# Performance work log

Measured on AMD Instinct MI355X. Metric: run time of the kernel, lower is better.

Reference implementation:

```python
import jax, jax.numpy as jnp
import numpy as np

B, S, D = 16, 1024, 1024

def _xavier_uniform(key, shape, fan_in, fan_out):
    a = float(np.sqrt(6.0 / (fan_in + fan_out)))
    return jax.random.uniform(key, shape, jnp.float32, -a, a)

def setup_inputs() -> dict:
    key = jax.random.key(0)
    ks = jax.random.split(key, 8)
    query = jax.random.normal(ks[0], (B, S, D), jnp.float32)
    key_t = jax.random.normal(ks[1], (B, S, D), jnp.float32)
    value = jax.random.normal(ks[2], (B, S, D), jnp.float32)
    # learned additive attention bias [1, S, S], xavier_uniform init
    attn_bias = _xavier_uniform(ks[3], (1, S, S), S, S)
    # Linear weights (torch nn.Linear default: kaiming-uniform-ish; any init ok for baseline)
    Wq = _xavier_uniform(ks[4], (D, D), D, D)
    bq = jnp.zeros((D,), jnp.float32)
    Wk = _xavier_uniform(ks[5], (D, D), D, D)
    bk = jnp.zeros((D,), jnp.float32)
    return {"query": query, "key": key_t, "value": value,
            "attn_bias": attn_bias, "Wq": Wq, "bq": bq, "Wk": Wk, "bk": bk}

def reference(query, key, value, attn_bias, Wq, bq, Wk, bk):
    # q = query @ Wq^T + bq  (torch Linear convention)
    q = jnp.einsum('bsd,ed->bse', query, Wq) + bq            # [B,S,D]
    k = jnp.einsum('bsd,ed->bse', key, Wk) + bk              # [B,S,D]
    energy = jnp.einsum('bsd,btd->bst', q, k) + attn_bias    # [B,S,S] (bias broadcasts over B)
    attention = jax.nn.softmax(energy, axis=-1)
    out = jnp.einsum('bst,btd->bsd', attention, value)       # value is NOT projected (matches source)
    return (out, attention)
```

## Files before the change

### kernel.cpp

```cpp
#include <hip/hip_runtime.h>


#define AS1 __attribute__((address_space(1)))
#define AS3 __attribute__((address_space(3)))
#define VMCNT(n) asm volatile("s_waitcnt vmcnt(" #n ")" ::: "memory")
#define SBARRIER asm volatile("s_barrier" ::: "memory")

typedef __bf16 bf16;
typedef __bf16 bf16x4 __attribute__((ext_vector_type(4)));
typedef __bf16 bf16x8 __attribute__((ext_vector_type(8)));
typedef float  f32x4  __attribute__((ext_vector_type(4)));

constexpr int BATCH = 16;
constexpr int S = 1024;
constexpr int D = 1024;
constexpr long NBSD = (long)BATCH * S * D;

constexpr int GBM = 256, GBN = 256, GBK = 32;
constexpr int NTK = 1024 / GBK;
constexpr int ARR = GBM * GBK;

__device__ __forceinline__ void stage16(const bf16* src, const bf16* dst) {
  __builtin_amdgcn_global_load_lds((const AS1 void*)src, (AS3 void*)dst, 16, 0, 0);
}

__global__ __launch_bounds__(256) void split_convert(
    const float* __restrict__ in, bf16* __restrict__ hi, bf16* __restrict__ lo, int n4) {
  int i = blockIdx.x * blockDim.x + threadIdx.x;
  int stride = gridDim.x * blockDim.x;
  for (; i < n4; i += stride) {
    f32x4 x = ((const f32x4*)in)[i];
    bf16x4 h, l;
#pragma unroll
    for (int j = 0; j < 4; ++j) {
      float v = x[j];
      bf16 hh = (bf16)v;
      h[j] = hh;
      l[j] = (bf16)(v - (float)hh);
    }
    ((bf16x4*)hi)[i] = h;
    ((bf16x4*)lo)[i] = l;
  }
}

__global__ __launch_bounds__(256) void transpose_convert(
    const float* __restrict__ v, bf16* __restrict__ vT) {
  __shared__ float tile[32][33];
  const int b = blockIdx.z;
  const int t0 = blockIdx.y * 32, d0 = blockIdx.x * 32;
  const int tx = threadIdx.x & 31, ty = threadIdx.x >> 5;
  const float* src = v + (long)b * S * D;
#pragma unroll
  for (int i = 0; i < 4; ++i)
    tile[ty + i * 8][tx] = src[(long)(t0 + ty + i * 8) * D + d0 + tx];
  __syncthreads();
  bf16* dst = vT + (long)b * D * S;
#pragma unroll
  for (int i = 0; i < 4; ++i)
    dst[(long)(d0 + ty + i * 8) * S + t0 + tx] = (bf16)tile[tx][ty + i * 8];
}

template <int EPI>
__global__ __launch_bounds__(512, 2) void gemm8_split(
    const bf16* __restrict__ Ah_g, const bf16* __restrict__ Al_g, long a_bs,
    const bf16* __restrict__ Bh_g, const bf16* __restrict__ Bl_g, long b_bs,
    const float* __restrict__ bias,
    bf16* __restrict__ Ch, bf16* __restrict__ Cl,
    float* __restrict__ Cf, long c_bs) {
  __shared__ bf16 lds[2 * 4 * ARR];

  const int tid = threadIdx.x;
  const int lane = tid & 63, wid = tid >> 6;
  const int wr = wid >> 2, wc = wid & 3;
  const int fr = lane & 15, fq = lane >> 4;
  const int fsw = (fr >> 1) & 3;

  const int w = blockIdx.x;
  const int swz = (w & 7) * 32 + (w >> 3);
  int z, by, bx;
  if constexpr (EPI == 0) { z = 0; by = swz >> 2; bx = swz & 3; }
  else { z = swz >> 4; by = (swz >> 2) & 3; bx = swz & 3; }
  const long brow = (long)by * GBM, bcol = (long)bx * GBN;

  const bf16* A_h = Ah_g + (long)z * a_bs;
  const bf16* A_l = Al_g + (long)z * a_bs;
  const bf16* B_h = Bh_g + (long)z * b_bs;
  const bf16* B_l = Bl_g + (long)z * b_bs;

  const int srow = tid >> 2;
  const int csw = ((tid & 3) ^ ((srow >> 1) & 3)) * 8;
  const long asrc = (brow + srow) * 1024 + csw;
  const long bsrc = (bcol + srow) * 1024 + csw;
  const int dstoff = wid * 512;

  const int aoffb = (wr * 128 + fr) * 32 + (fq ^ fsw) * 8;
  const int boffb = (wc * 64 + fr) * 32 + (fq ^ fsw) * 8;

  f32x4 acc[8][4] = {};

#define STG(slot, arr, base, koff, rr) \
  stage16((base) + (koff) + (long)(rr) * 131072, \
          lds + ((slot) * 4 + (arr)) * ARR + (rr) * 4096 + dstoff)

  STG(0, 0, A_h + asrc, 0, 0); STG(0, 0, A_h + asrc, 0, 1);
  STG(0, 2, B_h + bsrc, 0, 0); STG(0, 2, B_h + bsrc, 0, 1);
  STG(0, 3, B_l + bsrc, 0, 0); STG(0, 3, B_l + bsrc, 0, 1);
  STG(0, 1, A_l + asrc, 0, 0); STG(0, 1, A_l + asrc, 0, 1);

  for (int t = 0; t < NTK; ++t) {
    const int cur = t & 1, nxt = cur ^ 1;
    const bf16* lA_h = lds + (cur * 4 + 0) * ARR;
    const bf16* lA_l = lds + (cur * 4 + 1) * ARR;
    const bf16* lB_h = lds + (cur * 4 + 2) * ARR;
    const bf16* lB_l = lds + (cur * 4 + 3) * ARR;

    if (t + 1 < NTK) {
      const long kn = (long)(t + 1) * GBK;
      STG(nxt, 0, A_h + asrc, kn, 0); STG(nxt, 0, A_h + asrc, kn, 1);
      STG(nxt, 2, B_h + bsrc, kn, 0); STG(nxt, 2, B_h + bsrc, kn, 1);
      STG(nxt, 3, B_l + bsrc, kn, 0); STG(nxt, 3, B_l + bsrc, kn, 1);
      STG(nxt, 1, A_l + asrc, kn, 0); STG(nxt, 1, A_l + asrc, kn, 1);
      VMCNT(8);
    } else {
      VMCNT(0);
    }
    __builtin_amdgcn_sched_barrier(0);
    SBARRIER;

    bf16x8 ah[8], bh[4];
#pragma unroll
    for (int m = 0; m < 8; ++m) ah[m] = *(const bf16x8*)&lA_h[aoffb + m * 512];
#pragma unroll
    for (int n = 0; n < 4; ++n) bh[n] = *(const bf16x8*)&lB_h[boffb + n * 512];
#pragma unroll
    for (int n = 0; n < 4; ++n)
#pragma unroll
      for (int m = 0; m < 8; ++m)
        acc[m][n] = __builtin_amdgcn_mfma_f32_16x16x32_bf16(ah[m], bh[n], acc[m][n], 0, 0, 0);

    bf16x8 bl[4];
#pragma unroll
    for (int n = 0; n < 4; ++n) bl[n] = *(const bf16x8*)&lB_l[boffb + n * 512];
#pragma unroll
    for (int n = 0; n < 4; ++n)
#pragma unroll
      for (int m = 0; m < 8; ++m)
        acc[m][n] = __builtin_amdgcn_mfma_f32_16x16x32_bf16(ah[m], bl[n], acc[m][n], 0, 0, 0);

    bf16x8 al[8];
#pragma unroll
    for (int m = 0; m < 8; ++m) al[m] = *(const bf16x8*)&lA_l[aoffb + m * 512];
#pragma unroll
    for (int n = 0; n < 4; ++n)
#pragma unroll
      for (int m = 0; m < 8; ++m)
        acc[m][n] = __builtin_amdgcn_mfma_f32_16x16x32_bf16(al[m], bh[n], acc[m][n], 0, 0, 0);

    SBARRIER;
  }
#undef STG

  if constexpr (EPI == 0) {
#pragma unroll
    for (int n = 0; n < 4; ++n) {
      const long col = bcol + wc * 64 + n * 16 + fr;
      const float bv = bias[col];
#pragma unroll
      for (int m = 0; m < 8; ++m) {
        const long row0 = brow + wr * 128 + m * 16 + fq * 4;
#pragma unroll
        for (int j = 0; j < 4; ++j) {
          const float c = acc[m][n][j] + bv;
          const bf16 h = (bf16)c;
          const bf16 l = (bf16)(c - (float)h);
          const long idx = (row0 + j) * 1024 + col;
          Ch[idx] = h;
          Cl[idx] = l;
        }
      }
    }
  } else {
    float* Cz = Cf + (long)z * c_bs;
#pragma unroll
    for (int n = 0; n < 4; ++n) {
      const long col = bcol + wc * 64 + n * 16 + fr;
#pragma unroll
      for (int m = 0; m < 8; ++m) {
        const long row0 = brow + wr * 128 + m * 16 + fq * 4;
#pragma unroll
        for (int j = 0; j < 4; ++j) {
          const long row = row0 + j;
          Cz[row * 1024 + col] = acc[m][n][j] + bias[row * 1024 + col];
        }
      }
    }
  }
}

__global__ __launch_bounds__(512, 2) void gemm8_plain(
    const bf16* __restrict__ A_g, long a_bs,
    const bf16* __restrict__ B_g, long b_bs,
    float* __restrict__ C, long c_bs) {
  __shared__ bf16 lds[2 * 2 * ARR];

  const int tid = threadIdx.x;
  const int lane = tid & 63, wid = tid >> 6;
  const int wr = wid >> 2, wc = wid & 3;
  const int fr = lane & 15, fq = lane >> 4;
  const int fsw = (fr >> 1) & 3;

  const int w = blockIdx.x;
  const int swz = (w & 7) * 32 + (w >> 3);
  const int z = swz >> 4, by = (swz >> 2) & 3, bx = swz & 3;
  const long brow = (long)by * GBM, bcol = (long)bx * GBN;

  const bf16* A = A_g + (long)z * a_bs;
  const bf16* B = B_g + (long)z * b_bs;

  const int srow = tid >> 2;
  const int csw = ((tid & 3) ^ ((srow >> 1) & 3)) * 8;
  const long asrc = (brow + srow) * 1024 + csw;
  const long bsrc = (bcol + srow) * 1024 + csw;
  const int dstoff = wid * 512;

  const int aoffb = (wr * 128 + fr) * 32 + (fq ^ fsw) * 8;
  const int boffb = (wc * 64 + fr) * 32 + (fq ^ fsw) * 8;

  f32x4 acc[8][4] = {};

#define STG2(slot, arr, base, koff, rr) \
  stage16((base) + (koff) + (long)(rr) * 131072, \
          lds + ((slot) * 2 + (arr)) * ARR + (rr) * 4096 + dstoff)

  STG2(0, 0, A + asrc, 0, 0); STG2(0, 0, A + asrc, 0, 1);
  STG2(0, 1, B + bsrc, 0, 0); STG2(0, 1, B + bsrc, 0, 1);

  for (int t = 0; t < NTK; ++t) {
    const int cur = t & 1, nxt = cur ^ 1;
    const bf16* lA = lds + (cur * 2 + 0) * ARR;
    const bf16* lB = lds + (cur * 2 + 1) * ARR;

    if (t + 1 < NTK) {
      const long kn = (long)(t + 1) * GBK;
      STG2(nxt, 0, A + asrc, kn, 0); STG2(nxt, 0, A + asrc, kn, 1);
      STG2(nxt, 1, B + bsrc, kn, 0); STG2(nxt, 1, B + bsrc, kn, 1);
      VMCNT(4);
    } else {
      VMCNT(0);
    }
    __builtin_amdgcn_sched_barrier(0);
    SBARRIER;

    bf16x8 ah[8], bh[4];
#pragma unroll
    for (int m = 0; m < 8; ++m) ah[m] = *(const bf16x8*)&lA[aoffb + m * 512];
#pragma unroll
    for (int n = 0; n < 4; ++n) bh[n] = *(const bf16x8*)&lB[boffb + n * 512];
#pragma unroll
    for (int n = 0; n < 4; ++n)
#pragma unroll
      for (int m = 0; m < 8; ++m)
        acc[m][n] = __builtin_amdgcn_mfma_f32_16x16x32_bf16(ah[m], bh[n], acc[m][n], 0, 0, 0);

    SBARRIER;
  }
#undef STG2

  float* Cz = C + (long)z * c_bs;
#pragma unroll
  for (int n = 0; n < 4; ++n) {
    const long col = bcol + wc * 64 + n * 16 + fr;
#pragma unroll
    for (int m = 0; m < 8; ++m) {
      const long row0 = brow + wr * 128 + m * 16 + fq * 4;
#pragma unroll
      for (int j = 0; j < 4; ++j)
        Cz[(row0 + j) * 1024 + col] = acc[m][n][j];
    }
  }
}

__global__ __launch_bounds__(256) void softmax_rows(
    float* __restrict__ attn, bf16* __restrict__ attn_bf) {
  const long row = blockIdx.x;
  float* p = attn + row * 1024;
  const int tid = threadIdx.x, lane = tid & 63, wid = tid >> 6;

  f32x4 x = ((const f32x4*)p)[tid];
  float m = fmaxf(fmaxf(x[0], x[1]), fmaxf(x[2], x[3]));
#pragma unroll
  for (int off = 32; off; off >>= 1) m = fmaxf(m, __shfl_xor(m, off));
  __shared__ float redm[4];
  if (lane == 0) redm[wid] = m;
  __syncthreads();
  m = fmaxf(fmaxf(redm[0], redm[1]), fmaxf(redm[2], redm[3]));

  f32x4 e;
#pragma unroll
  for (int j = 0; j < 4; ++j) e[j] = __expf(x[j] - m);
  float s = e[0] + e[1] + e[2] + e[3];
#pragma unroll
  for (int off = 32; off; off >>= 1) s += __shfl_xor(s, off);
  __shared__ float reds[4];
  if (lane == 0) reds[wid] = s;
  __syncthreads();
  s = reds[0] + reds[1] + reds[2] + reds[3];

  const float inv = 1.0f / s;
  f32x4 r;
  bf16x4 rb;
#pragma unroll
  for (int j = 0; j < 4; ++j) {
    r[j] = e[j] * inv;
    rb[j] = (bf16)r[j];
  }
  ((f32x4*)p)[tid] = r;
  ((bf16x4*)(attn_bf + row * 1024))[tid] = rb;
}

extern "C" void kernel_launch(void* const* d_in, const int* in_sizes, int n_in,
                              void* d_out, int out_size, void* d_ws, size_t ws_size,
                              hipStream_t stream) {
  const float* query     = (const float*)d_in[0];
  const float* key       = (const float*)d_in[1];
  const float* value     = (const float*)d_in[2];
  const float* attn_bias = (const float*)d_in[3];
  const float* Wq        = (const float*)d_in[4];
  const float* bq        = (const float*)d_in[5];
  const float* Wk        = (const float*)d_in[6];
  const float* bk        = (const float*)d_in[7];

  float* out  = (float*)d_out;
  float* attn = out + NBSD;

  bf16* ws    = (bf16*)d_ws;
  bf16* q_hi  = ws;
  bf16* q_lo  = ws + NBSD;
  bf16* k_hi  = ws + 2 * NBSD;
  bf16* k_lo  = ws + 3 * NBSD;
  bf16* Wq_hi = ws + 4 * NBSD;
  bf16* Wq_lo = Wq_hi + (long)D * D;
  bf16* Wk_hi = Wq_lo + (long)D * D;
  bf16* Wk_lo = Wk_hi + (long)D * D;
  bf16* scr   = Wk_lo + (long)D * D;
  bf16* key_hi = scr;
  bf16* key_lo = scr + NBSD;
  bf16* valueT  = scr;
  bf16* attn_bf = scr + NBSD;
  bf16* query_hi = (bf16*)d_out;
  bf16* query_lo = query_hi + NBSD;

  split_convert<<<2048, 256, 0, stream>>>(query, query_hi, query_lo, (int)(NBSD / 4));
  split_convert<<<2048, 256, 0, stream>>>(key, key_hi, key_lo, (int)(NBSD / 4));
  split_convert<<<512, 256, 0, stream>>>(Wq, Wq_hi, Wq_lo, D * D / 4);
  split_convert<<<512, 256, 0, stream>>>(Wk, Wk_hi, Wk_lo, D * D / 4);

  gemm8_split<0><<<256, 512, 0, stream>>>(query_hi, query_lo, 0, Wq_hi, Wq_lo, 0,
                                          bq, q_hi, q_lo, nullptr, 0);
  gemm8_split<0><<<256, 512, 0, stream>>>(key_hi, key_lo, 0, Wk_hi, Wk_lo, 0,
                                          bk, k_hi, k_lo, nullptr, 0);

  transpose_convert<<<dim3(32, 32, 16), 256, 0, stream>>>(value, valueT);

  gemm8_split<1><<<256, 512, 0, stream>>>(q_hi, q_lo, (long)S * D, k_hi, k_lo, (long)S * D,
                                          attn_bias, nullptr, nullptr, attn, (long)S * S);

  softmax_rows<<<BATCH * S, 256, 0, stream>>>(attn, attn_bf);

  gemm8_plain<<<256, 512, 0, stream>>>(attn_bf, (long)S * S, valueT, (long)D * S,
                                       out, (long)S * D);
}
```

Measured before the change: 480.8 us.

## Interleave LDS reads, global prefetch and MFMA clusters in split-bf16 projection GEMM

The projection GEMM's K loop used to stage all next-tile data at the top, then read LDS and issue three blocks of MFMAs. It is now broken into six MFMA clusters, with per-cluster s_setprio and fine-grained lgkmcnt/vmcnt waits. Each cluster overlaps partial LDS fragment loads and a slice of the next tile's global-to-LDS copies, and the next tile's A_h/B_h fragments are preloaded across the loop boundary. The aim is to hide LDS and global latency behind matrix-core work, at the cost of more barriers per iteration and a more fragile wait-count schedule.

```diff
diff --git a/kernel.cpp b/kernel.cpp
--- a/kernel.cpp
+++ b/kernel.cpp
@@ -4,7 +4,9 @@
 #define AS1 __attribute__((address_space(1)))
 #define AS3 __attribute__((address_space(3)))
 #define VMCNT(n) asm volatile("s_waitcnt vmcnt(" #n ")" ::: "memory")
+#define LGKM(n)  asm volatile("s_waitcnt lgkmcnt(" #n ")" ::: "memory")
 #define SBARRIER asm volatile("s_barrier" ::: "memory")
+#define SB0 __builtin_amdgcn_sched_barrier(0)
 
 typedef __bf16 bf16;
 typedef __bf16 bf16x4 __attribute__((ext_vector_type(4)));
@@ -97,68 +99,91 @@
   const int boffb = (wc * 64 + fr) * 32 + (fq ^ fsw) * 8;
 
   f32x4 acc[8][4] = {};
+  bf16x8 ah[8], al[8], bh[4], bl[4];
 
 #define STG(slot, arr, base, koff, rr) \
   stage16((base) + (koff) + (long)(rr) * 131072, \
           lds + ((slot) * 4 + (arr)) * ARR + (rr) * 4096 + dstoff)
+
+#define CLUSTER(AF, BF, N0) \
+  __builtin_amdgcn_s_setprio(1); \
+  _Pragma("unroll") \
+  for (int m = 0; m < 8; ++m) \
+    acc[m][N0] = __builtin_amdgcn_mfma_f32_16x16x32_bf16(AF[m], BF[N0], acc[m][N0], 0, 0, 0); \
+  _Pragma("unroll") \
+  for (int m = 0; m < 8; ++m) \
+    acc[m][N0+1] = __builtin_amdgcn_mfma_f32_16x16x32_bf16(AF[m], BF[N0+1], acc[m][N0+1], 0, 0, 0); \
+  __builtin_amdgcn_s_setprio(0)
 
   STG(0, 0, A_h + asrc, 0, 0); STG(0, 0, A_h + asrc, 0, 1);
   STG(0, 2, B_h + bsrc, 0, 0); STG(0, 2, B_h + bsrc, 0, 1);
   STG(0, 3, B_l + bsrc, 0, 0); STG(0, 3, B_l + bsrc, 0, 1);
   STG(0, 1, A_l + asrc, 0, 0); STG(0, 1, A_l + asrc, 0, 1);
+  VMCNT(4);
+  SBARRIER;
+  {
+    const bf16* lA_h0 = lds;
+    const bf16* lB_h0 = lds + 2 * ARR;
+#pragma unroll
+    for (int m = 0; m < 8; ++m) ah[m] = *(const bf16x8*)&lA_h0[aoffb + m * 512];
+    bh[0] = *(const bf16x8*)&lB_h0[boffb];
+    bh[1] = *(const bf16x8*)&lB_h0[boffb + 512];
+  }
 
   for (int t = 0; t < NTK; ++t) {
     const int cur = t & 1, nxt = cur ^ 1;
-    const bf16* lA_h = lds + (cur * 4 + 0) * ARR;
+    const long kn = (long)(t + 1) * GBK;
+    const bool pf = (t + 1 < NTK);
     const bf16* lA_l = lds + (cur * 4 + 1) * ARR;
     const bf16* lB_h = lds + (cur * 4 + 2) * ARR;
     const bf16* lB_l = lds + (cur * 4 + 3) * ARR;
-
-    if (t + 1 < NTK) {
-      const long kn = (long)(t + 1) * GBK;
+    const bf16* nA_h = lds + (nxt * 4 + 0) * ARR;
+    const bf16* nB_h = lds + (nxt * 4 + 2) * ARR;
+
+    bh[2] = *(const bf16x8*)&lB_h[boffb + 2 * 512];
+    bh[3] = *(const bf16x8*)&lB_h[boffb + 3 * 512];
+    if (pf) {
       STG(nxt, 0, A_h + asrc, kn, 0); STG(nxt, 0, A_h + asrc, kn, 1);
-      STG(nxt, 2, B_h + bsrc, kn, 0); STG(nxt, 2, B_h + bsrc, kn, 1);
-      STG(nxt, 3, B_l + bsrc, kn, 0); STG(nxt, 3, B_l + bsrc, kn, 1);
-      STG(nxt, 1, A_l + asrc, kn, 0); STG(nxt, 1, A_l + asrc, kn, 1);
-      VMCNT(8);
+      VMCNT(2);
     } else {
       VMCNT(0);
     }
-    __builtin_amdgcn_sched_barrier(0);
-    SBARRIER;
-
-    bf16x8 ah[8], bh[4];
-#pragma unroll
-    for (int m = 0; m < 8; ++m) ah[m] = *(const bf16x8*)&lA_h[aoffb + m * 512];
-#pragma unroll
-    for (int n = 0; n < 4; ++n) bh[n] = *(const bf16x8*)&lB_h[boffb + n * 512];
-#pragma unroll
-    for (int n = 0; n < 4; ++n)
-#pragma unroll
-      for (int m = 0; m < 8; ++m)
-        acc[m][n] = __builtin_amdgcn_mfma_f32_16x16x32_bf16(ah[m], bh[n], acc[m][n], 0, 0, 0);
-
-    bf16x8 bl[4];
-#pragma unroll
-    for (int n = 0; n < 4; ++n) bl[n] = *(const bf16x8*)&lB_l[boffb + n * 512];
-#pragma unroll
-    for (int n = 0; n < 4; ++n)
-#pragma unroll
-      for (int m = 0; m < 8; ++m)
-        acc[m][n] = __builtin_amdgcn_mfma_f32_16x16x32_bf16(ah[m], bl[n], acc[m][n], 0, 0, 0);
-
-    bf16x8 al[8];
+    SBARRIER; LGKM(2); SB0;
+    CLUSTER(ah, bh, 0);
+
+    bl[0] = *(const bf16x8*)&lB_l[boffb];
+    bl[1] = *(const bf16x8*)&lB_l[boffb + 512];
+    if (pf) { STG(nxt, 2, B_h + bsrc, kn, 0); STG(nxt, 2, B_h + bsrc, kn, 1); }
+    SBARRIER; LGKM(2); SB0;
+    CLUSTER(ah, bh, 2);
+
+    bl[2] = *(const bf16x8*)&lB_l[boffb + 2 * 512];
+    bl[3] = *(const bf16x8*)&lB_l[boffb + 3 * 512];
+    if (pf) { STG(nxt, 3, B_l + bsrc, kn, 0); STG(nxt, 3, B_l + bsrc, kn, 1); }
+    SBARRIER; LGKM(2); SB0;
+    CLUSTER(ah, bl, 0);
+
 #pragma unroll
     for (int m = 0; m < 8; ++m) al[m] = *(const bf16x8*)&lA_l[aoffb + m * 512];
-#pragma unroll
-    for (int n = 0; n < 4; ++n)
-#pragma unroll
-      for (int m = 0; m < 8; ++m)
-        acc[m][n] = __builtin_amdgcn_mfma_f32_16x16x32_bf16(al[m], bh[n], acc[m][n], 0, 0, 0);
-
-    SBARRIER;
+    if (pf) { STG(nxt, 1, A_l + asrc, kn, 0); STG(nxt, 1, A_l + asrc, kn, 1); }
+    SBARRIER; LGKM(8); SB0;
+    CLUSTER(ah, bl, 2);
+
+    if (pf) { VMCNT(4); } else { VMCNT(0); }
+    SBARRIER; LGKM(0); SB0;
+    CLUSTER(al, bh, 0);
+
+    if (pf) {
+#pragma unroll
+      for (int m = 0; m < 8; ++m) ah[m] = *(const bf16x8*)&nA_h[aoffb + m * 512];
+      bh[0] = *(const bf16x8*)&nB_h[boffb];
+      bh[1] = *(const bf16x8*)&nB_h[boffb + 512];
+    }
+    SBARRIER; SB0;
+    CLUSTER(al, bh, 2);
   }
 #undef STG
+#undef CLUSTER
 
   if constexpr (EPI == 0) {
 #pragma unroll
@@ -248,7 +273,7 @@
     } else {
       VMCNT(0);
     }
-    __builtin_amdgcn_sched_barrier(0);
+    SB0;
     SBARRIER;
 
     bf16x8 ah[8], bh[4];
```

Result: faster. 460.6 us (-4.2%).

## Switch split-bf16 GEMM to 32x32x16 MFMA with per-phase staged prefetch

Applied to the files above, without the earlier changes.

Rewrites the three-pass split-bf16 GEMM to use 32x32x16 MFMA tiles instead of 16x16x32, which cuts LDS fragment reads per MFMA. It also staggers the next tile's global-to-LDS prefetch across the three hi/lo MFMA phases, with finer vmcnt/lgkmcnt waits and barriers, and raises wave priority around the MFMA clusters. The aim is better MFMA throughput and overlap of loads with compute. It adds more barriers per k-step and changes the register footprint.

```diff
diff --git a/kernel.cpp b/kernel.cpp
--- a/kernel.cpp
+++ b/kernel.cpp
@@ -4,12 +4,15 @@
 #define AS1 __attribute__((address_space(1)))
 #define AS3 __attribute__((address_space(3)))
 #define VMCNT(n) asm volatile("s_waitcnt vmcnt(" #n ")" ::: "memory")
+#define LGKM(n)  asm volatile("s_waitcnt lgkmcnt(" #n ")" ::: "memory")
 #define SBARRIER asm volatile("s_barrier" ::: "memory")
+#define SB0 __builtin_amdgcn_sched_barrier(0)
 
 typedef __bf16 bf16;
 typedef __bf16 bf16x4 __attribute__((ext_vector_type(4)));
 typedef __bf16 bf16x8 __attribute__((ext_vector_type(8)));
 typedef float  f32x4  __attribute__((ext_vector_type(4)));
+typedef float  f32x16 __attribute__((ext_vector_type(16)));
 
 constexpr int BATCH = 16;
 constexpr int S = 1024;
@@ -61,7 +64,7 @@
 }
 
 template <int EPI>
-__global__ __launch_bounds__(512, 2) void gemm8_split(
+__global__ __launch_bounds__(512, 2) void gemm32_split(
     const bf16* __restrict__ Ah_g, const bf16* __restrict__ Al_g, long a_bs,
     const bf16* __restrict__ Bh_g, const bf16* __restrict__ Bl_g, long b_bs,
     const float* __restrict__ bias,
@@ -72,8 +75,8 @@
   const int tid = threadIdx.x;
   const int lane = tid & 63, wid = tid >> 6;
   const int wr = wid >> 2, wc = wid & 3;
-  const int fr = lane & 15, fq = lane >> 4;
-  const int fsw = (fr >> 1) & 3;
+  const int lr = lane & 31;
+  const int lk = lane >> 5;
 
   const int w = blockIdx.x;
   const int swz = (w & 7) * 32 + (w >> 3);
@@ -93,87 +96,119 @@
   const long bsrc = (bcol + srow) * 1024 + csw;
   const int dstoff = wid * 512;
 
-  const int aoffb = (wr * 128 + fr) * 32 + (fq ^ fsw) * 8;
-  const int boffb = (wc * 64 + fr) * 32 + (fq ^ fsw) * 8;
-
-  f32x4 acc[8][4] = {};
+  int aoff[4][2], boff[2][2];
+#pragma unroll
+  for (int i = 0; i < 4; ++i) {
+    const int r = wr * 128 + i * 32 + lr;
+#pragma unroll
+    for (int s = 0; s < 2; ++s)
+      aoff[i][s] = r * 32 + (((2 * s + lk) ^ ((r >> 1) & 3)) * 8);
+  }
+#pragma unroll
+  for (int j = 0; j < 2; ++j) {
+    const int r = wc * 64 + j * 32 + lr;
+#pragma unroll
+    for (int s = 0; s < 2; ++s)
+      boff[j][s] = r * 32 + (((2 * s + lk) ^ ((r >> 1) & 3)) * 8);
+  }
+
+  f32x16 acc[4][2] = {};
+  bf16x8 ah[4][2], al[4][2], bh[2][2], bl[2][2];
 
 #define STG(slot, arr, base, koff, rr) \
   stage16((base) + (koff) + (long)(rr) * 131072, \
           lds + ((slot) * 4 + (arr)) * ARR + (rr) * 4096 + dstoff)
+
+#define CLUSTER(AF, BF) \
+  __builtin_amdgcn_s_setprio(1); \
+  _Pragma("unroll") \
+  for (int s = 0; s < 2; ++s) \
+    _Pragma("unroll") \
+    for (int i = 0; i < 4; ++i) \
+      _Pragma("unroll") \
+      for (int j = 0; j < 2; ++j) \
+        acc[i][j] = __builtin_amdgcn_mfma_f32_32x32x16_bf16(AF[i][s], BF[j][s], acc[i][j], 0, 0, 0); \
+  __builtin_amdgcn_s_setprio(0)
 
   STG(0, 0, A_h + asrc, 0, 0); STG(0, 0, A_h + asrc, 0, 1);
   STG(0, 2, B_h + bsrc, 0, 0); STG(0, 2, B_h + bsrc, 0, 1);
   STG(0, 3, B_l + bsrc, 0, 0); STG(0, 3, B_l + bsrc, 0, 1);
   STG(0, 1, A_l + asrc, 0, 0); STG(0, 1, A_l + asrc, 0, 1);
+  VMCNT(4);
+  SBARRIER;
 
   for (int t = 0; t < NTK; ++t) {
     const int cur = t & 1, nxt = cur ^ 1;
+    const long kn = (long)(t + 1) * GBK;
+    const bool pf = (t + 1 < NTK);
     const bf16* lA_h = lds + (cur * 4 + 0) * ARR;
     const bf16* lA_l = lds + (cur * 4 + 1) * ARR;
     const bf16* lB_h = lds + (cur * 4 + 2) * ARR;
     const bf16* lB_l = lds + (cur * 4 + 3) * ARR;
 
-    if (t + 1 < NTK) {
-      const long kn = (long)(t + 1) * GBK;
+#pragma unroll
+    for (int i = 0; i < 4; ++i)
+#pragma unroll
+      for (int s = 0; s < 2; ++s) ah[i][s] = *(const bf16x8*)&lA_h[aoff[i][s]];
+#pragma unroll
+    for (int j = 0; j < 2; ++j)
+#pragma unroll
+      for (int s = 0; s < 2; ++s) bh[j][s] = *(const bf16x8*)&lB_h[boff[j][s]];
+    if (pf) {
       STG(nxt, 0, A_h + asrc, kn, 0); STG(nxt, 0, A_h + asrc, kn, 1);
       STG(nxt, 2, B_h + bsrc, kn, 0); STG(nxt, 2, B_h + bsrc, kn, 1);
+      VMCNT(6);
+    } else {
+      VMCNT(2);
+    }
+    SBARRIER; LGKM(0); SB0;
+    CLUSTER(ah, bh);
+    SBARRIER;
+
+#pragma unroll
+    for (int j = 0; j < 2; ++j)
+#pragma unroll
+      for (int s = 0; s < 2; ++s) bl[j][s] = *(const bf16x8*)&lB_l[boff[j][s]];
+    if (pf) {
       STG(nxt, 3, B_l + bsrc, kn, 0); STG(nxt, 3, B_l + bsrc, kn, 1);
-      STG(nxt, 1, A_l + asrc, kn, 0); STG(nxt, 1, A_l + asrc, kn, 1);
-      VMCNT(8);
+      VMCNT(6);
     } else {
       VMCNT(0);
     }
-    __builtin_amdgcn_sched_barrier(0);
+    SBARRIER; LGKM(0); SB0;
+    CLUSTER(ah, bl);
     SBARRIER;
 
-    bf16x8 ah[8], bh[4];
-#pragma unroll
-    for (int m = 0; m < 8; ++m) ah[m] = *(const bf16x8*)&lA_h[aoffb + m * 512];
-#pragma unroll
-    for (int n = 0; n < 4; ++n) bh[n] = *(const bf16x8*)&lB_h[boffb + n * 512];
-#pragma unroll
-    for (int n = 0; n < 4; ++n)
-#pragma unroll
-      for (int m = 0; m < 8; ++m)
-        acc[m][n] = __builtin_amdgcn_mfma_f32_16x16x32_bf16(ah[m], bh[n], acc[m][n], 0, 0, 0);
-
-    bf16x8 bl[4];
-#pragma unroll
-    for (int n = 0; n < 4; ++n) bl[n] = *(const bf16x8*)&lB_l[boffb + n * 512];
-#pragma unroll
-    for (int n = 0; n < 4; ++n)
-#pragma unroll
-      for (int m = 0; m < 8; ++m)
-        acc[m][n] = __builtin_amdgcn_mfma_f32_16x16x32_bf16(ah[m], bl[n], acc[m][n], 0, 0, 0);
-
-    bf16x8 al[8];
-#pragma unroll
-    for (int m = 0; m < 8; ++m) al[m] = *(const bf16x8*)&lA_l[aoffb + m * 512];
-#pragma unroll
-    for (int n = 0; n < 4; ++n)
-#pragma unroll
-      for (int m = 0; m < 8; ++m)
-        acc[m][n] = __builtin_amdgcn_mfma_f32_16x16x32_bf16(al[m], bh[n], acc[m][n], 0, 0, 0);
-
+#pragma unroll
+    for (int i = 0; i < 4; ++i)
+#pragma unroll
+      for (int s = 0; s < 2; ++s) al[i][s] = *(const bf16x8*)&lA_l[aoff[i][s]];
+    if (pf) {
+      STG(nxt, 1, A_l + asrc, kn, 0); STG(nxt, 1, A_l + asrc, kn, 1);
+      VMCNT(4);
+    }
+    SBARRIER; LGKM(0); SB0;
+    CLUSTER(al, bh);
     SBARRIER;
   }
 #undef STG
+#undef CLUSTER
 
   if constexpr (EPI == 0) {
 #pragma unroll
-    for (int n = 0; n < 4; ++n) {
-      const long col = bcol + wc * 64 + n * 16 + fr;
+    for (int j = 0; j < 2; ++j) {
+      const long col = bcol + wc * 64 + j * 32 + lr;
       const float bv = bias[col];
 #pragma unroll
-      for (int m = 0; m < 8; ++m) {
-        const long row0 = brow + wr * 128 + m * 16 + fq * 4;
-#pragma unroll
-        for (int j = 0; j < 4; ++j) {
-          const float c = acc[m][n][j] + bv;
+      for (int i = 0; i < 4; ++i) {
+        const long row0 = brow + wr * 128 + i * 32 + 4 * lk;
+#pragma unroll
+        for (int r = 0; r < 16; ++r) {
+          const long row = row0 + (r & 3) + 8 * (r >> 2);
+          const float c = acc[i][j][r] + bv;
           const bf16 h = (bf16)c;
           const bf16 l = (bf16)(c - (float)h);
-          const long idx = (row0 + j) * 1024 + col;
+          const long idx = row * 1024 + col;
           Ch[idx] = h;
           Cl[idx] = l;
         }
@@ -182,15 +217,15 @@
   } else {
     float* Cz = Cf + (long)z * c_bs;
 #pragma unroll
-    for (int n = 0; n < 4; ++n) {
-      const long col = bcol + wc * 64 + n * 16 + fr;
-#pragma unroll
-      for (int m = 0; m < 8; ++m) {
-        const long row0 = brow + wr * 128 + m * 16 + fq * 4;
-#pragma unroll
-        for (int j = 0; j < 4; ++j) {
-          const long row = row0 + j;
-          Cz[row * 1024 + col] = acc[m][n][j] + bias[row * 1024 + col];
+    for (int j = 0; j < 2; ++j) {
+      const long col = bcol + wc * 64 + j * 32 + lr;
+#pragma unroll
+      for (int i = 0; i < 4; ++i) {
+        const long row0 = brow + wr * 128 + i * 32 + 4 * lk;
+#pragma unroll
+        for (int r = 0; r < 16; ++r) {
+          const long row = row0 + (r & 3) + 8 * (r >> 2);
+          Cz[row * 1024 + col] = acc[i][j][r] + bias[row * 1024 + col];
         }
       }
     }
@@ -248,7 +283,7 @@
     } else {
       VMCNT(0);
     }
-    __builtin_amdgcn_sched_barrier(0);
+    SB0;
     SBARRIER;
 
     bf16x8 ah[8], bh[4];
@@ -355,15 +390,15 @@
   split_convert<<<512, 256, 0, stream>>>(Wq, Wq_hi, Wq_lo, D * D / 4);
   split_convert<<<512, 256, 0, stream>>>(Wk, Wk_hi, Wk_lo, D * D / 4);
 
-  gemm8_split<0><<<256, 512, 0, stream>>>(query_hi, query_lo, 0, Wq_hi, Wq_lo, 0,
-                                          bq, q_hi, q_lo, nullptr, 0);
-  gemm8_split<0><<<256, 512, 0, stream>>>(key_hi, key_lo, 0, Wk_hi, Wk_lo, 0,
-                                          bk, k_hi, k_lo, nullptr, 0);
+  gemm32_split<0><<<256, 512, 0, stream>>>(query_hi, query_lo, 0, Wq_hi, Wq_lo, 0,
+                                           bq, q_hi, q_lo, nullptr, 0);
+  gemm32_split<0><<<256, 512, 0, stream>>>(key_hi, key_lo, 0, Wk_hi, Wk_lo, 0,
+                                           bk, k_hi, k_lo, nullptr, 0);
 
   transpose_convert<<<dim3(32, 32, 16), 256, 0, stream>>>(value, valueT);
 
-  gemm8_split<1><<<256, 512, 0, stream>>>(q_hi, q_lo, (long)S * D, k_hi, k_lo, (long)S * D,
-                                          attn_bias, nullptr, nullptr, attn, (long)S * S);
+  gemm32_split<1><<<256, 512, 0, stream>>>(q_hi, q_lo, (long)S * D, k_hi, k_lo, (long)S * D,
+                                           attn_bias, nullptr, nullptr, attn, (long)S * S);
 
   softmax_rows<<<BATCH * S, 256, 0, stream>>>(attn, attn_bf);
 
```

After: 438.3 us (median of 2 runs). 8.8% less time.

## Rewrite GEMMs as unified 4-phase pipelined kernel with K=64 tiles

Applied to the files above, without the earlier changes.

Replaces the split and plain GEMM kernels with one templated kernel. It concatenates the hi/lo split products along an extended K dimension (NREG regions of 16 K-tiles of 64) instead of doing three MFMA passes per tile. Each K-tile is split into four sub-phases that interleave LDS fragment reads, staged global-to-LDS prefetches one and two tiles ahead, and MFMA blocks raised with s_setprio. The LDS layout and XOR swizzle change for 64-wide K rows. The goal is better overlap of memory and compute and fewer idle barriers. The cost is one block per CU from launch_bounds(512,1), more barriers per tile, and larger register pressure.

```diff
diff --git a/kernel.cpp b/kernel.cpp
--- a/kernel.cpp
+++ b/kernel.cpp
@@ -4,7 +4,9 @@
 #define AS1 __attribute__((address_space(1)))
 #define AS3 __attribute__((address_space(3)))
 #define VMCNT(n) asm volatile("s_waitcnt vmcnt(" #n ")" ::: "memory")
+#define LGKM(n)  asm volatile("s_waitcnt lgkmcnt(" #n ")" ::: "memory")
 #define SBARRIER asm volatile("s_barrier" ::: "memory")
+#define SB0 __builtin_amdgcn_sched_barrier(0)
 
 typedef __bf16 bf16;
 typedef __bf16 bf16x4 __attribute__((ext_vector_type(4)));
@@ -15,10 +17,6 @@
 constexpr int S = 1024;
 constexpr int D = 1024;
 constexpr long NBSD = (long)BATCH * S * D;
-
-constexpr int GBM = 256, GBN = 256, GBK = 32;
-constexpr int NTK = 1024 / GBK;
-constexpr int ARR = GBM * GBK;
 
 __device__ __forceinline__ void stage16(const bf16* src, const bf16* dst) {
   __builtin_amdgcn_global_load_lds((const AS1 void*)src, (AS3 void*)dst, 16, 0, 0);
@@ -60,105 +58,113 @@
     dst[(long)(d0 + ty + i * 8) * S + t0 + tx] = (bf16)tile[tx][ty + i * 8];
 }
 
-template <int EPI>
-__global__ __launch_bounds__(512, 2) void gemm8_split(
-    const bf16* __restrict__ Ah_g, const bf16* __restrict__ Al_g, long a_bs,
-    const bf16* __restrict__ Bh_g, const bf16* __restrict__ Bl_g, long b_bs,
+template <int EPI, int NREG>
+__global__ __launch_bounds__(512, 1) void gemm_p4(
+    const bf16* __restrict__ A0g, const bf16* __restrict__ A1g,
+    const bf16* __restrict__ A2g, long a_bs,
+    const bf16* __restrict__ B0g, const bf16* __restrict__ B1g,
+    const bf16* __restrict__ B2g, long b_bs,
     const float* __restrict__ bias,
     bf16* __restrict__ Ch, bf16* __restrict__ Cl,
     float* __restrict__ Cf, long c_bs) {
-  __shared__ bf16 lds[2 * 4 * ARR];
+  constexpr int NT = NREG * 16;
+  __shared__ bf16 lds[2][2][2][8192];
 
   const int tid = threadIdx.x;
   const int lane = tid & 63, wid = tid >> 6;
   const int wr = wid >> 2, wc = wid & 3;
   const int fr = lane & 15, fq = lane >> 4;
-  const int fsw = (fr >> 1) & 3;
 
   const int w = blockIdx.x;
   const int swz = (w & 7) * 32 + (w >> 3);
   int z, by, bx;
   if constexpr (EPI == 0) { z = 0; by = swz >> 2; bx = swz & 3; }
   else { z = swz >> 4; by = (swz >> 2) & 3; bx = swz & 3; }
-  const long brow = (long)by * GBM, bcol = (long)bx * GBN;
-
-  const bf16* A_h = Ah_g + (long)z * a_bs;
-  const bf16* A_l = Al_g + (long)z * a_bs;
-  const bf16* B_h = Bh_g + (long)z * b_bs;
-  const bf16* B_l = Bl_g + (long)z * b_bs;
-
-  const int srow = tid >> 2;
-  const int csw = ((tid & 3) ^ ((srow >> 1) & 3)) * 8;
-  const long asrc = (brow + srow) * 1024 + csw;
-  const long bsrc = (bcol + srow) * 1024 + csw;
-  const int dstoff = wid * 512;
-
-  const int aoffb = (wr * 128 + fr) * 32 + (fq ^ fsw) * 8;
-  const int boffb = (wc * 64 + fr) * 32 + (fq ^ fsw) * 8;
+  const long brow = (long)by * 256, bcol = (long)bx * 256;
+
+  const bf16* A0 = A0g + (long)z * a_bs;
+  const bf16* A1 = A1g + (long)z * a_bs;
+  const bf16* A2 = A2g + (long)z * a_bs;
+  const bf16* B0 = B0g + (long)z * b_bs;
+  const bf16* B1 = B1g + (long)z * b_bs;
+  const bf16* B2 = B2g + (long)z * b_bs;
+
+  auto APTR = [&](int t) -> const bf16* {
+    const int r = t >> 4; return r == 0 ? A0 : (r == 1 ? A1 : A2);
+  };
+  auto BPTR = [&](int t) -> const bf16* {
+    const int r = t >> 4; return r == 0 ? B0 : (r == 1 ? B1 : B2);
+  };
+
+  const int srow64 = tid >> 3;
+  const int scol = ((tid & 7) ^ (srow64 & 7)) * 8;
+
+  const int c0 = (((fq ^ (fr & 3)) | (((fr >> 2) & 1) << 2))) * 8;
+  const int arow = fr * 64;
+  const int brow_ = (wc & 1) * 4096 + fr * 64;
 
   f32x4 acc[8][4] = {};
-
-#define STG(slot, arr, base, koff, rr) \
-  stage16((base) + (koff) + (long)(rr) * 131072, \
-          lds + ((slot) * 4 + (arr)) * ARR + (rr) * 4096 + dstoff)
-
-  STG(0, 0, A_h + asrc, 0, 0); STG(0, 0, A_h + asrc, 0, 1);
-  STG(0, 2, B_h + bsrc, 0, 0); STG(0, 2, B_h + bsrc, 0, 1);
-  STG(0, 3, B_l + bsrc, 0, 0); STG(0, 3, B_l + bsrc, 0, 1);
-  STG(0, 1, A_l + asrc, 0, 0); STG(0, 1, A_l + asrc, 0, 1);
-
-  for (int t = 0; t < NTK; ++t) {
-    const int cur = t & 1, nxt = cur ^ 1;
-    const bf16* lA_h = lds + (cur * 4 + 0) * ARR;
-    const bf16* lA_l = lds + (cur * 4 + 1) * ARR;
-    const bf16* lB_h = lds + (cur * 4 + 2) * ARR;
-    const bf16* lB_l = lds + (cur * 4 + 3) * ARR;
-
-    if (t + 1 < NTK) {
-      const long kn = (long)(t + 1) * GBK;
-      STG(nxt, 0, A_h + asrc, kn, 0); STG(nxt, 0, A_h + asrc, kn, 1);
-      STG(nxt, 2, B_h + bsrc, kn, 0); STG(nxt, 2, B_h + bsrc, kn, 1);
-      STG(nxt, 3, B_l + bsrc, kn, 0); STG(nxt, 3, B_l + bsrc, kn, 1);
-      STG(nxt, 1, A_l + asrc, kn, 0); STG(nxt, 1, A_l + asrc, kn, 1);
-      VMCNT(8);
-    } else {
-      VMCNT(0);
-    }
-    __builtin_amdgcn_sched_barrier(0);
+  bf16x8 afr[4][2], bfr[4][2];
+
+#define STG(ARR, H, T) do { \
+    const bf16* _s = ((ARR) ? BPTR(T) : APTR(T)) + \
+      (((ARR) ? bcol : brow) + (H) * 128 + srow64) * 1024 + ((T) & 15) * 64 + scol; \
+    const bf16* _d = &lds[(T) & 1][ARR][H][wid * 512]; \
+    stage16(_s, _d); stage16(_s + 65536, _d + 4096); \
+  } while (0)
+
+#define RD_A() { const bf16* p = &lds[kt & 1][0][wr][0]; \
+    _Pragma("unroll") for (int m = 0; m < 4; ++m) { \
+      afr[m][0] = *(const bf16x8*)&p[(MBASE + m) * 1024 + arow + c0]; \
+      afr[m][1] = *(const bf16x8*)&p[(MBASE + m) * 1024 + arow + (c0 ^ 32)]; } }
+
+#define RD_B(N0) { const bf16* p = &lds[kt & 1][1][wc >> 1][0]; \
+    _Pragma("unroll") for (int n = 0; n < 2; ++n) { \
+      bfr[N0 + n][0] = *(const bf16x8*)&p[(N0 + n) * 1024 + brow_ + c0]; \
+      bfr[N0 + n][1] = *(const bf16x8*)&p[(N0 + n) * 1024 + brow_ + (c0 ^ 32)]; } }
+
+#define MM(M0, N0) \
+    __builtin_amdgcn_s_setprio(1); \
+    _Pragma("unroll") for (int kk = 0; kk < 2; ++kk) \
+      _Pragma("unroll") for (int m = 0; m < 4; ++m) \
+        _Pragma("unroll") for (int n = 0; n < 2; ++n) \
+          acc[M0 + m][N0 + n] = __builtin_amdgcn_mfma_f32_16x16x32_bf16( \
+              afr[m][kk], bfr[N0 + n][kk], acc[M0 + m][N0 + n], 0, 0, 0); \
+    __builtin_amdgcn_s_setprio(0)
+
+  STG(0, 0, 0); STG(0, 1, 0); STG(1, 0, 0); STG(1, 1, 0);
+  STG(1, 0, 1); STG(0, 0, 1);
+  VMCNT(4);
+  SBARRIER;
+
+  for (int kt = 0; kt < NT; ++kt) {
+    const bool p1 = kt + 1 < NT, p2 = kt + 2 < NT;
+    { constexpr int MBASE = 0; RD_A(); }
+    RD_B(0);
+    if (p1) STG(0, 1, kt + 1);
+    LGKM(0); SB0;
+    MM(0, 0);
     SBARRIER;
-
-    bf16x8 ah[8], bh[4];
-#pragma unroll
-    for (int m = 0; m < 8; ++m) ah[m] = *(const bf16x8*)&lA_h[aoffb + m * 512];
-#pragma unroll
-    for (int n = 0; n < 4; ++n) bh[n] = *(const bf16x8*)&lB_h[boffb + n * 512];
-#pragma unroll
-    for (int n = 0; n < 4; ++n)
-#pragma unroll
-      for (int m = 0; m < 8; ++m)
-        acc[m][n] = __builtin_amdgcn_mfma_f32_16x16x32_bf16(ah[m], bh[n], acc[m][n], 0, 0, 0);
-
-    bf16x8 bl[4];
-#pragma unroll
-    for (int n = 0; n < 4; ++n) bl[n] = *(const bf16x8*)&lB_l[boffb + n * 512];
-#pragma unroll
-    for (int n = 0; n < 4; ++n)
-#pragma unroll
-      for (int m = 0; m < 8; ++m)
-        acc[m][n] = __builtin_amdgcn_mfma_f32_16x16x32_bf16(ah[m], bl[n], acc[m][n], 0, 0, 0);
-
-    bf16x8 al[8];
-#pragma unroll
-    for (int m = 0; m < 8; ++m) al[m] = *(const bf16x8*)&lA_l[aoffb + m * 512];
-#pragma unroll
-    for (int n = 0; n < 4; ++n)
-#pragma unroll
-      for (int m = 0; m < 8; ++m)
-        acc[m][n] = __builtin_amdgcn_mfma_f32_16x16x32_bf16(al[m], bh[n], acc[m][n], 0, 0, 0);
-
+    RD_B(2);
+    if (p1) STG(1, 1, kt + 1);
+    LGKM(0); SB0;
+    MM(0, 2);
+    SBARRIER;
+    { constexpr int MBASE = 4; RD_A(); }
+    if (p2) STG(1, 0, kt + 2);
+    LGKM(0); SB0;
+    MM(4, 0);
+    SBARRIER;
+    if (p2) { STG(0, 0, kt + 2); VMCNT(4); }
+    else if (p1) { VMCNT(0); }
+    SB0;
+    MM(4, 2);
     SBARRIER;
   }
 #undef STG
+#undef RD_A
+#undef RD_B
+#undef MM
 
   if constexpr (EPI == 0) {
 #pragma unroll
@@ -179,7 +185,7 @@
         }
       }
     }
-  } else {
+  } else if constexpr (EPI == 1) {
     float* Cz = Cf + (long)z * c_bs;
 #pragma unroll
     for (int n = 0; n < 4; ++n) {
@@ -194,88 +200,18 @@
         }
       }
     }
-  }
-}
-
-__global__ __launch_bounds__(512, 2) void gemm8_plain(
-    const bf16* __restrict__ A_g, long a_bs,
-    const bf16* __restrict__ B_g, long b_bs,
-    float* __restrict__ C, long c_bs) {
-  __shared__ bf16 lds[2 * 2 * ARR];
-
-  const int tid = threadIdx.x;
-  const int lane = tid & 63, wid = tid >> 6;
-  const int wr = wid >> 2, wc = wid & 3;
-  const int fr = lane & 15, fq = lane >> 4;
-  const int fsw = (fr >> 1) & 3;
-
-  const int w = blockIdx.x;
-  const int swz = (w & 7) * 32 + (w >> 3);
-  const int z = swz >> 4, by = (swz >> 2) & 3, bx = swz & 3;
-  const long brow = (long)by * GBM, bcol = (long)bx * GBN;
-
-  const bf16* A = A_g + (long)z * a_bs;
-  const bf16* B = B_g + (long)z * b_bs;
-
-  const int srow = tid >> 2;
-  const int csw = ((tid & 3) ^ ((srow >> 1) & 3)) * 8;
-  const long asrc = (brow + srow) * 1024 + csw;
-  const long bsrc = (bcol + srow) * 1024 + csw;
-  const int dstoff = wid * 512;
-
-  const int aoffb = (wr * 128 + fr) * 32 + (fq ^ fsw) * 8;
-  const int boffb = (wc * 64 + fr) * 32 + (fq ^ fsw) * 8;
-
-  f32x4 acc[8][4] = {};
-
-#define STG2(slot, arr, base, koff, rr) \
-  stage16((base) + (koff) + (long)(rr) * 131072, \
-          lds + ((slot) * 2 + (arr)) * ARR + (rr) * 4096 + dstoff)
-
-  STG2(0, 0, A + asrc, 0, 0); STG2(0, 0, A + asrc, 0, 1);
-  STG2(0, 1, B + bsrc, 0, 0); STG2(0, 1, B + bsrc, 0, 1);
-
-  for (int t = 0; t < NTK; ++t) {
-    const int cur = t & 1, nxt = cur ^ 1;
-    const bf16* lA = lds + (cur * 2 + 0) * ARR;
-    const bf16* lB = lds + (cur * 2 + 1) * ARR;
-
-    if (t + 1 < NTK) {
-      const long kn = (long)(t + 1) * GBK;
-      STG2(nxt, 0, A + asrc, kn, 0); STG2(nxt, 0, A + asrc, kn, 1);
-      STG2(nxt, 1, B + bsrc, kn, 0); STG2(nxt, 1, B + bsrc, kn, 1);
-      VMCNT(4);
-    } else {
-      VMCNT(0);
-    }
-    __builtin_amdgcn_sched_barrier(0);
-    SBARRIER;
-
-    bf16x8 ah[8], bh[4];
-#pragma unroll
-    for (int m = 0; m < 8; ++m) ah[m] = *(const bf16x8*)&lA[aoffb + m * 512];
-#pragma unroll
-    for (int n = 0; n < 4; ++n) bh[n] = *(const bf16x8*)&lB[boffb + n * 512];
-#pragma unroll
-    for (int n = 0; n < 4; ++n)
-#pragma unroll
-      for (int m = 0; m < 8; ++m)
-        acc[m][n] = __builtin_amdgcn_mfma_f32_16x16x32_bf16(ah[m], bh[n], acc[m][n], 0, 0, 0);
-
-    SBARRIER;
-  }
-#undef STG2
-
-  float* Cz = C + (long)z * c_bs;
-#pragma unroll
-  for (int n = 0; n < 4; ++n) {
-    const long col = bcol + wc * 64 + n * 16 + fr;
-#pragma unroll
-    for (int m = 0; m < 8; ++m) {
-      const long row0 = brow + wr * 128 + m * 16 + fq * 4;
-#pragma unroll
-      for (int j = 0; j < 4; ++j)
-        Cz[(row0 + j) * 1024 + col] = acc[m][n][j];
+  } else {
+    float* Cz = Cf + (long)z * c_bs;
+#pragma unroll
+    for (int n = 0; n < 4; ++n) {
+      const long col = bcol + wc * 64 + n * 16 + fr;
+#pragma unroll
+      for (int m = 0; m < 8; ++m) {
+        const long row0 = brow + wr * 128 + m * 16 + fq * 4;
+#pragma unroll
+        for (int j = 0; j < 4; ++j)
+          Cz[(row0 + j) * 1024 + col] = acc[m][n][j];
+      }
     }
   }
 }
@@ -355,18 +291,22 @@
   split_convert<<<512, 256, 0, stream>>>(Wq, Wq_hi, Wq_lo, D * D / 4);
   split_convert<<<512, 256, 0, stream>>>(Wk, Wk_hi, Wk_lo, D * D / 4);
 
-  gemm8_split<0><<<256, 512, 0, stream>>>(query_hi, query_lo, 0, Wq_hi, Wq_lo, 0,
-                                          bq, q_hi, q_lo, nullptr, 0);
-  gemm8_split<0><<<256, 512, 0, stream>>>(key_hi, key_lo, 0, Wk_hi, Wk_lo, 0,
-                                          bk, k_hi, k_lo, nullptr, 0);
+  gemm_p4<0, 3><<<256, 512, 0, stream>>>(query_hi, query_hi, query_lo, 0,
+                                         Wq_hi, Wq_lo, Wq_hi, 0,
+                                         bq, q_hi, q_lo, nullptr, 0);
+  gemm_p4<0, 3><<<256, 512, 0, stream>>>(key_hi, key_hi, key_lo, 0,
+                                         Wk_hi, Wk_lo, Wk_hi, 0,
+                                         bk, k_hi, k_lo, nullptr, 0);
 
   transpose_convert<<<dim3(32, 32, 16), 256, 0, stream>>>(value, valueT);
 
-  gemm8_split<1><<<256, 512, 0, stream>>>(q_hi, q_lo, (long)S * D, k_hi, k_lo, (long)S * D,
-                                          attn_bias, nullptr, nullptr, attn, (long)S * S);
+  gemm_p4<1, 3><<<256, 512, 0, stream>>>(q_hi, q_hi, q_lo, (long)S * D,
+                                         k_hi, k_lo, k_hi, (long)S * D,
+                                         attn_bias, nullptr, nullptr, attn, (long)S * S);
 
   softmax_rows<<<BATCH * S, 256, 0, stream>>>(attn, attn_bf);
 
-  gemm8_plain<<<256, 512, 0, stream>>>(attn_bf, (long)S * S, valueT, (long)D * S,
-                                       out, (long)S * D);
-}
+  gemm_p4<2, 1><<<256, 512, 0, stream>>>(attn_bf, attn_bf, attn_bf, (long)S * S,
+                                         valueT, valueT, valueT, (long)D * S,
+                                         nullptr, nullptr, nullptr, out, (long)S * D);
+}
```

After: 473.0 us. Within noise of the previous version (-1.6%).
